# Kernel tuning notes

Hardware: AMD Instinct MI355X
Metric: run time of the kernel (lower is better)

## Reference

```python
import jax, jax.numpy as jnp
import numpy as np

B, S, D_IN, D_HID, D_OUT, PE_DIM = 8, 4096, 1024, 1024, 1024, 16


def sinusoidal_embeddings(batch_size, seq_len, dim):
    positions = jnp.arange(seq_len)[:, None].astype(jnp.float32)
    div_term = jnp.exp(jnp.arange(0, dim, 2).astype(jnp.float32) * (-jnp.log(10000.0) / dim))
    pe = jnp.zeros((seq_len, dim), dtype=jnp.float32)
    pe = pe.at[:, 0::2].set(jnp.sin(positions * div_term))
    pe = pe.at[:, 1::2].set(jnp.cos(positions * div_term))
    return jnp.broadcast_to(pe, (batch_size, seq_len, dim))


def setup_inputs() -> dict:
    key = jax.random.key(0)
    ks = jax.random.split(key, 8)
    d_cat = D_IN + PE_DIM
    # a_logit drawn so that sigmoid(a_logit) lands in the stable decay range [0.9, 0.999]
    u = jax.random.uniform(ks[1], (D_HID,), minval=0.9, maxval=0.999)
    a_logit = jnp.log(u) - jnp.log1p(-u)  # logit
    scale_in = 1.0 / np.sqrt(d_cat)
    scale_h = 1.0 / np.sqrt(D_HID)
    return {
        "x": jax.random.normal(ks[0], (B, S, D_IN), dtype=jnp.float32),
        "a_logit": a_logit.astype(jnp.float32),
        "W_dx": jax.random.normal(ks[2], (d_cat, D_OUT), dtype=jnp.float32) * scale_in,
        "b_dx": jnp.zeros((D_OUT,), dtype=jnp.float32),
        "W_in": jax.random.normal(ks[3], (d_cat, D_HID), dtype=jnp.float32) * scale_in,
        "b_in": jnp.zeros((D_HID,), dtype=jnp.float32),
        "W_out": jax.random.normal(ks[4], (D_HID, D_OUT), dtype=jnp.float32) * scale_h,
        "b_out": jnp.zeros((D_OUT,), dtype=jnp.float32),
    }


def reference(x, a_logit, W_dx, b_dx, W_in, b_in, W_out, b_out):
    batch, seq, _ = x.shape
    a = jax.nn.sigmoid(a_logit)  # (d_hidden,)
    # rnn_pos_embedding: concat 16-dim sinusoidal PE
    xc = jnp.concatenate([x, sinusoidal_embeddings(batch, seq, PE_DIM)], axis=-1)
    dx = xc @ W_dx + b_dx  # (B, S, d_out)
    u = xc @ W_in + b_in  # (B, S, d_hidden)
    # rnn_norm_input
    u = jnp.sqrt(1.0 - a ** 2) * u
    u = jnp.transpose(u, (1, 0, 2))  # (S, B, d_hidden)

    def step(h, xt):
        h = a * h + xt
        return h, h

    init = jnp.zeros((batch, a.shape[0]), dtype=x.dtype)
    _, h = jax.lax.scan(step, init, u)
    h = jnp.transpose(h, (1, 0, 2))  # (B, S, d_hidden)
    return (dx + h @ W_out + b_out) / 2
```

## Files before the change

kernel.cpp:

```cpp
#include <hip/hip_runtime.h>
#include <hip/hip_bf16.h>
#include <math.h>

#define B_DIM 8
#define S_DIM 4096
#define DIN   1024
#define DHID  1024
#define DOUT  1024
#define KCAT  1040
#define KC    1088
#define MTOT  (B_DIM*S_DIM)
#define NCHUNK 32
#define LCHUNK 128

typedef __attribute__((ext_vector_type(8))) short bf16x8;
typedef __attribute__((ext_vector_type(4))) float f32x4;
typedef __attribute__((ext_vector_type(4))) unsigned short u16x4;

__device__ __forceinline__ unsigned short f2bf(float f) {
  union { float f; unsigned u; } v; v.f = f;
  unsigned r = v.u + 0x7fffu + ((v.u >> 16) & 1u);
  return (unsigned short)(r >> 16);
}
__device__ __forceinline__ float bf2f(unsigned short h) {
  union { unsigned u; float f; } v; v.u = ((unsigned)h) << 16;
  return v.f;
}

#define GLOAD16(g, l)                                                         \
  __builtin_amdgcn_global_load_lds(                                           \
      (const __attribute__((address_space(1))) void*)(g),                     \
      (__attribute__((address_space(3))) void*)(l), 16, 0, 0)

#define BAR()   __builtin_amdgcn_s_barrier()
#define LGKM0() do { asm volatile("s_waitcnt lgkmcnt(0)" ::: "memory");       \
                     __builtin_amdgcn_sched_barrier(0); } while (0)


__global__ void prep_a_kernel(const float* __restrict__ logit,
                              float* __restrict__ avec, float* __restrict__ svec) {
  int d = blockIdx.x * 256 + threadIdx.x;
  if (d >= DHID) return;
  float a = 1.f / (1.f + expf(-logit[d]));
  avec[d] = a;
  svec[d] = sqrtf(fmaxf(0.f, 1.f - a * a));
}

__global__ __launch_bounds__(256) void transpose_cast_kernel(
    const float* __restrict__ W, unsigned short* __restrict__ Wt,
    int Ksrc, int KCdst) {
  __shared__ float tile[32][33];
  const int N = 1024;
  int kb = blockIdx.x * 32, nb = blockIdx.y * 32;
  int tx = threadIdx.x & 31, ty = threadIdx.x >> 5;
#pragma unroll
  for (int r = 0; r < 32; r += 8) {
    int k = kb + ty + r;
    tile[ty + r][tx] = (k < Ksrc) ? W[(size_t)k * N + nb + tx] : 0.f;
  }
  __syncthreads();
#pragma unroll
  for (int r = 0; r < 32; r += 8) {
    int n = nb + ty + r;
    Wt[(size_t)n * KCdst + kb + tx] = f2bf(tile[tx][ty + r]);
  }
}

__global__ __launch_bounds__(256) void build_xc_kernel(
    const float* __restrict__ x, unsigned short* __restrict__ xc) {
  int gid = blockIdx.x * 256 + threadIdx.x;
  if (gid >= MTOT * (KC / 4)) return;
  int row = gid / (KC / 4);
  int g = gid - row * (KC / 4);
  int col0 = g * 4;
  u16x4 val;
  if (col0 < DIN) {
    const float4 xv = *(const float4*)(x + (size_t)row * DIN + col0);
    val.x = f2bf(xv.x); val.y = f2bf(xv.y); val.z = f2bf(xv.z); val.w = f2bf(xv.w);
  } else {
    int t = row & (S_DIM - 1);
#pragma unroll
    for (int e = 0; e < 4; e++) {
      int col = col0 + e;
      float v = 0.f;
      if (col < KCAT) {
        int j = col - DIN;
        int i = j >> 1;
        float div = expf(-(float)i * 1.1512925465f);
        float arg = (float)t * div;
        v = (j & 1) ? cosf(arg) : sinf(arg);
      }
      val[e] = f2bf(v);
    }
  }
  *(u16x4*)(xc + (size_t)row * KC + col0) = val;
}


__device__ __forceinline__ bf16x8 frag(const unsigned short* hb, int row, int slot) {
  int ph = slot ^ (row & 7);
  return *(const bf16x8*)(hb + (size_t)row * 64 + ph * 8);
}

__device__ __forceinline__ void gemm_pipe2(
    const unsigned short* __restrict__ A,
    const unsigned short* __restrict__ Bt,
    int lda, int kt, int arow0, int brow0,
    unsigned short (*lA)[2][8192], unsigned short (*lB)[2][8192],
    f32x4 acc[8][4]) {
  const int tid = threadIdx.x;
  const int lane = tid & 63, w = tid >> 6;
  const int wrow = w >> 2, wcol = w & 3;
  const int rl = lane & 15, s = lane >> 4;

  const int c1 = tid, c2 = tid + 512;
  const int r1 = c1 >> 3, sl1 = (c1 & 7) ^ (r1 & 7);
  const int r2 = c2 >> 3, sl2 = (c2 & 7) ^ (r2 & 7);
  const unsigned short* pA1 = A + (size_t)(arow0 + r1) * lda + sl1 * 8;
  const unsigned short* pA2 = A + (size_t)(arow0 + r2) * lda + sl2 * 8;
  const unsigned short* pB1 = Bt + (size_t)(brow0 + r1) * lda + sl1 * 8;
  const unsigned short* pB2 = Bt + (size_t)(brow0 + r2) * lda + sl2 * 8;
  const size_t hstep = (size_t)128 * lda;

#define STG_A(t, h) do { size_t _o = (size_t)(t) * 64 + (size_t)(h) * hstep;  \
    int _b = (t) & 1;                                                         \
    GLOAD16(pA1 + _o, &lA[_b][h][(size_t)c1 * 8]);                            \
    GLOAD16(pA2 + _o, &lA[_b][h][(size_t)c2 * 8]); } while (0)
#define STG_B(t, h) do { size_t _o = (size_t)(t) * 64 + (size_t)(h) * hstep;  \
    int _b = (t) & 1;                                                         \
    GLOAD16(pB1 + _o, &lB[_b][h][(size_t)c1 * 8]);                            \
    GLOAD16(pB2 + _o, &lB[_b][h][(size_t)c2 * 8]); } while (0)

#define MFMA_Q(MH, NH, BB)                                                    \
  __builtin_amdgcn_s_setprio(1);                                              \
  _Pragma("unroll") for (int mq = 0; mq < 4; mq++)                            \
    _Pragma("unroll") for (int nq = 0; nq < 2; nq++)                          \
      _Pragma("unroll") for (int kk = 0; kk < 2; kk++)                        \
        acc[(MH)*4 + mq][(NH)*2 + nq] =                                       \
            __builtin_amdgcn_mfma_f32_16x16x32_bf16(                          \
                a[mq][kk], BB[nq][kk], acc[(MH)*4 + mq][(NH)*2 + nq], 0, 0, 0);\
  __builtin_amdgcn_s_setprio(0);

  STG_B(0, 0); STG_B(0, 1); STG_A(0, 0); STG_A(0, 1);
  STG_B(1, 0); STG_B(1, 1); STG_A(1, 0); STG_A(1, 1);
  asm volatile("s_waitcnt vmcnt(8)" ::: "memory");
  BAR();

  const int br = (wcol & 1) * 64;
  for (int t = 0; t < kt; ++t) {
    const bool st = (t + 2) < kt;
    const unsigned short* Ac = &lA[t & 1][wrow][0];
    const unsigned short* Bc = &lB[t & 1][wcol >> 1][0];
    bf16x8 a[4][2], b0[2][2], b1[2][2];

#pragma unroll
    for (int mq = 0; mq < 4; mq++)
#pragma unroll
      for (int kk = 0; kk < 2; kk++)
        a[mq][kk] = frag(Ac, mq * 16 + rl, kk * 4 + s);
#pragma unroll
    for (int nq = 0; nq < 2; nq++)
#pragma unroll
      for (int kk = 0; kk < 2; kk++)
        b0[nq][kk] = frag(Bc, br + nq * 16 + rl, kk * 4 + s);
    BAR(); LGKM0();
    MFMA_Q(0, 0, b0);
    BAR();

#pragma unroll
    for (int nq = 0; nq < 2; nq++)
#pragma unroll
      for (int kk = 0; kk < 2; kk++)
        b1[nq][kk] = frag(Bc, br + 32 + nq * 16 + rl, kk * 4 + s);
    BAR(); LGKM0();
    MFMA_Q(0, 1, b1);
    BAR();

#pragma unroll
    for (int mq = 0; mq < 4; mq++)
#pragma unroll
      for (int kk = 0; kk < 2; kk++)
        a[mq][kk] = frag(Ac, 64 + mq * 16 + rl, kk * 4 + s);
    if (st) { STG_B(t + 2, 0); STG_B(t + 2, 1); }
    BAR(); LGKM0();
    MFMA_Q(1, 1, b1);
    BAR();

    if (st) { STG_A(t + 2, 0); STG_A(t + 2, 1); }
    BAR();
    MFMA_Q(1, 0, b0);
    if (st) { asm volatile("s_waitcnt vmcnt(8)" ::: "memory"); }
    else    { asm volatile("s_waitcnt vmcnt(0)" ::: "memory"); }
    BAR();
  }
#undef STG_A
#undef STG_B
#undef MFMA_Q
}

__global__ __launch_bounds__(512, 2) void gemm_u_kernel(
    const unsigned short* __restrict__ xc, const unsigned short* __restrict__ Wtin,
    const float* __restrict__ b_in, const float* __restrict__ svec,
    unsigned short* __restrict__ u) {
  __shared__ __align__(16) unsigned short lA[2][2][8192];
  __shared__ __align__(16) unsigned short lB[2][2][8192];
  f32x4 acc[8][4];
  const f32x4 z = {0.f, 0.f, 0.f, 0.f};
#pragma unroll
  for (int i = 0; i < 8; i++)
#pragma unroll
    for (int n = 0; n < 4; n++) acc[i][n] = z;

  int bid = blockIdx.x;
  int swz = (bid & 7) * 64 + (bid >> 3);
  int bcol = swz >> 7, brow = swz & 127;

  gemm_pipe2(xc, Wtin, KC, KC / 64, brow * 256, bcol * 256, lA, lB, acc);

  const int lane = threadIdx.x & 63, w = threadIdx.x >> 6;
  const int wrow = w >> 2, wcol = w & 3;
  const int rl = lane & 15, s = lane >> 4;
  const int colb = bcol * 256 + wcol * 64 + rl;
  const int rowb = brow * 256 + wrow * 128 + s * 4;
#pragma unroll
  for (int n = 0; n < 4; n++) {
    int col = colb + n * 16;
    float bi = b_in[col], sv = svec[col];
#pragma unroll
    for (int i = 0; i < 8; i++) {
#pragma unroll
      for (int r = 0; r < 4; r++) {
        int row = rowb + i * 16 + r;
        u[(size_t)row * DHID + col] = f2bf((acc[i][n][r] + bi) * sv);
      }
    }
  }
}

__global__ __launch_bounds__(512, 2) void gemm_out_kernel(
    const unsigned short* __restrict__ xc, const unsigned short* __restrict__ Wtdx,
    const unsigned short* __restrict__ h, const unsigned short* __restrict__ Wtout,
    const float* __restrict__ b_dx, const float* __restrict__ b_out,
    float* __restrict__ out) {
  __shared__ __align__(16) unsigned short lA[2][2][8192];
  __shared__ __align__(16) unsigned short lB[2][2][8192];
  f32x4 acc[8][4];
  const f32x4 z = {0.f, 0.f, 0.f, 0.f};
#pragma unroll
  for (int i = 0; i < 8; i++)
#pragma unroll
    for (int n = 0; n < 4; n++) acc[i][n] = z;

  int bid = blockIdx.x;
  int swz = (bid & 7) * 64 + (bid >> 3);
  int bcol = swz >> 7, brow = swz & 127;

  gemm_pipe2(xc, Wtdx, KC, KC / 64, brow * 256, bcol * 256, lA, lB, acc);
  gemm_pipe2(h, Wtout, DHID, DHID / 64, brow * 256, bcol * 256, lA, lB, acc);

  const int lane = threadIdx.x & 63, w = threadIdx.x >> 6;
  const int wrow = w >> 2, wcol = w & 3;
  const int rl = lane & 15, s = lane >> 4;
  const int colb = bcol * 256 + wcol * 64 + rl;
  const int rowb = brow * 256 + wrow * 128 + s * 4;
#pragma unroll
  for (int n = 0; n < 4; n++) {
    int col = colb + n * 16;
    float bb = b_dx[col] + b_out[col];
#pragma unroll
    for (int i = 0; i < 8; i++) {
#pragma unroll
      for (int r = 0; r < 4; r++) {
        int row = rowb + i * 16 + r;
        out[(size_t)row * DOUT + col] = 0.5f * (acc[i][n][r] + bb);
      }
    }
  }
}


__global__ __launch_bounds__(256) void scan1_kernel(
    const float* __restrict__ avec, unsigned short* __restrict__ uh,
    float* __restrict__ carry) {
  int b = blockIdx.x >> 5, c = blockIdx.x & 31;
  int d0 = threadIdx.x * 4;
  float4 a4 = *(const float4*)(avec + d0);
  unsigned short* p = uh + ((size_t)(b * S_DIM + c * LCHUNK)) * DHID + d0;
  float h0 = 0.f, h1 = 0.f, h2 = 0.f, h3 = 0.f;
#pragma unroll 4
  for (int t = 0; t < LCHUNK; t++) {
    u16x4 v = *(u16x4*)(p + (size_t)t * DHID);
    h0 = fmaf(a4.x, h0, bf2f(v.x));
    h1 = fmaf(a4.y, h1, bf2f(v.y));
    h2 = fmaf(a4.z, h2, bf2f(v.z));
    h3 = fmaf(a4.w, h3, bf2f(v.w));
    v.x = f2bf(h0); v.y = f2bf(h1); v.z = f2bf(h2); v.w = f2bf(h3);
    *(u16x4*)(p + (size_t)t * DHID) = v;
  }
  float4 cv = {h0, h1, h2, h3};
  *(float4*)(carry + ((size_t)b * NCHUNK + c) * DHID + d0) = cv;
}

__global__ __launch_bounds__(256) void scan2_kernel(
    const float* __restrict__ avec, const float* __restrict__ carry,
    float* __restrict__ Hprev) {
  int gid = blockIdx.x * 256 + threadIdx.x;
  int b = gid >> 10, d = gid & 1023;
  float a = avec[d];
  float aL = a;
#pragma unroll
  for (int i = 0; i < 7; i++) aL *= aL;
  float H = 0.f;
#pragma unroll
  for (int c = 0; c < NCHUNK; c++) {
    size_t idx = ((size_t)b * NCHUNK + c) * DHID + d;
    Hprev[idx] = H;
    H = aL * H + carry[idx];
  }
}

__global__ __launch_bounds__(256) void scan3_kernel(
    const float* __restrict__ avec, unsigned short* __restrict__ uh,
    const float* __restrict__ Hprev) {
  int b = blockIdx.x >> 5, c = blockIdx.x & 31;
  int d0 = threadIdx.x * 4;
  float4 Hp = *(const float4*)(Hprev + ((size_t)b * NCHUNK + c) * DHID + d0);
  if (Hp.x == 0.f && Hp.y == 0.f && Hp.z == 0.f && Hp.w == 0.f) return;
  float4 a4 = *(const float4*)(avec + d0);
  float p0 = a4.x * Hp.x, p1 = a4.y * Hp.y, p2 = a4.z * Hp.z, p3 = a4.w * Hp.w;
  unsigned short* p = uh + ((size_t)(b * S_DIM + c * LCHUNK)) * DHID + d0;
#pragma unroll 4
  for (int t = 0; t < LCHUNK; t++) {
    u16x4 v = *(u16x4*)(p + (size_t)t * DHID);
    v.x = f2bf(bf2f(v.x) + p0);
    v.y = f2bf(bf2f(v.y) + p1);
    v.z = f2bf(bf2f(v.z) + p2);
    v.w = f2bf(bf2f(v.w) + p3);
    *(u16x4*)(p + (size_t)t * DHID) = v;
    p0 *= a4.x; p1 *= a4.y; p2 *= a4.z; p3 *= a4.w;
  }
}


extern "C" void kernel_launch(void* const* d_in, const int* in_sizes, int n_in,
                              void* d_out, int out_size, void* d_ws, size_t ws_size,
                              hipStream_t stream) {
  const float* x       = (const float*)d_in[0];
  const float* a_logit = (const float*)d_in[1];
  const float* W_dx    = (const float*)d_in[2];
  const float* b_dx    = (const float*)d_in[3];
  const float* W_in    = (const float*)d_in[4];
  const float* b_in    = (const float*)d_in[5];
  const float* W_out   = (const float*)d_in[6];
  const float* b_out   = (const float*)d_in[7];
  float* out = (float*)d_out;

  char* ws = (char*)d_ws;
  size_t off = 0;
  auto alloc = [&](size_t bytes) {
    void* p = ws + off;
    off += (bytes + 255) & ~(size_t)255;
    return p;
  };
  unsigned short* xc    = (unsigned short*)alloc((size_t)MTOT * KC * 2);
  unsigned short* Wtdx  = (unsigned short*)alloc((size_t)DOUT * KC * 2);
  unsigned short* Wtin  = (unsigned short*)alloc((size_t)DHID * KC * 2);
  unsigned short* Wtout = (unsigned short*)alloc((size_t)DOUT * DHID * 2);
  unsigned short* uh    = (unsigned short*)alloc((size_t)MTOT * DHID * 2);
  float* carry = (float*)alloc((size_t)B_DIM * NCHUNK * DHID * 4);
  float* Hprev = (float*)alloc((size_t)B_DIM * NCHUNK * DHID * 4);
  float* avec  = (float*)alloc(DHID * 4);
  float* svec  = (float*)alloc(DHID * 4);
  (void)ws_size; (void)in_sizes; (void)n_in; (void)out_size;

  prep_a_kernel<<<4, 256, 0, stream>>>(a_logit, avec, svec);
  transpose_cast_kernel<<<dim3(KC / 32, 32), 256, 0, stream>>>(W_dx, Wtdx, KCAT, KC);
  transpose_cast_kernel<<<dim3(KC / 32, 32), 256, 0, stream>>>(W_in, Wtin, KCAT, KC);
  transpose_cast_kernel<<<dim3(32, 32), 256, 0, stream>>>(W_out, Wtout, DHID, DHID);
  build_xc_kernel<<<(MTOT * (KC / 4) + 255) / 256, 256, 0, stream>>>(x, xc);

  gemm_u_kernel<<<512, 512, 0, stream>>>(xc, Wtin, b_in, svec, uh);

  scan1_kernel<<<B_DIM * NCHUNK, 256, 0, stream>>>(avec, uh, carry);
  scan2_kernel<<<32, 256, 0, stream>>>(avec, carry, Hprev);
  scan3_kernel<<<B_DIM * NCHUNK, 256, 0, stream>>>(avec, uh, Hprev);

  gemm_out_kernel<<<512, 512, 0, stream>>>(xc, Wtdx, uh, Wtout, b_dx, b_out, out);
}
```

Before: 339.6 us.

## Restructure GEMM main loop with register prefetch and fused dual-GEMM pipeline

Result: slower. 356.1 us (+4.8%).

```diff
diff --git a/kernel.cpp b/kernel.cpp
--- a/kernel.cpp
+++ b/kernel.cpp
@@ -31,10 +31,6 @@
   __builtin_amdgcn_global_load_lds(                                           \
       (const __attribute__((address_space(1))) void*)(g),                     \
       (__attribute__((address_space(3))) void*)(l), 16, 0, 0)
-
-#define BAR()   __builtin_amdgcn_s_barrier()
-#define LGKM0() do { asm volatile("s_waitcnt lgkmcnt(0)" ::: "memory");       \
-                     __builtin_amdgcn_sched_barrier(0); } while (0)
 
 
 __global__ void prep_a_kernel(const float* __restrict__ logit,
@@ -102,100 +98,114 @@
   return *(const bf16x8*)(hb + (size_t)row * 64 + ph * 8);
 }
 
-__device__ __forceinline__ void gemm_pipe2(
-    const unsigned short* __restrict__ A,
-    const unsigned short* __restrict__ Bt,
-    int lda, int kt, int arow0, int brow0,
+#define READ_A(dst, base, roff)                                               \
+  _Pragma("unroll") for (int mq = 0; mq < 4; mq++)                            \
+    _Pragma("unroll") for (int kk = 0; kk < 2; kk++)                          \
+      dst[mq][kk] = frag(base, (roff) + mq * 16 + rl, kk * 4 + s);
+
+#define READ_B(dst, base, roff)                                               \
+  _Pragma("unroll") for (int nq = 0; nq < 2; nq++)                            \
+    _Pragma("unroll") for (int kk = 0; kk < 2; kk++)                          \
+      dst[nq][kk] = frag(base, (roff) + nq * 16 + rl, kk * 4 + s);
+
+#define MFMA_Q(MH, NH, AA, BB)                                                \
+  __builtin_amdgcn_s_setprio(1);                                              \
+  _Pragma("unroll") for (int mq = 0; mq < 4; mq++)                            \
+    _Pragma("unroll") for (int nq = 0; nq < 2; nq++)                          \
+      _Pragma("unroll") for (int kk = 0; kk < 2; kk++)                        \
+        acc[(MH)*4 + mq][(NH)*2 + nq] =                                       \
+            __builtin_amdgcn_mfma_f32_16x16x32_bf16(                          \
+                AA[mq][kk], BB[nq][kk], acc[(MH)*4 + mq][(NH)*2 + nq], 0,0,0);\
+  __builtin_amdgcn_s_setprio(0);
+
+__device__ __forceinline__ void gemm_pipe3(
+    const unsigned short* __restrict__ A0p, const unsigned short* __restrict__ B0p,
+    int lda0, int kt0,
+    const unsigned short* __restrict__ A1p, const unsigned short* __restrict__ B1p,
+    int lda1, int kt1,
+    int arow0, int brow0,
     unsigned short (*lA)[2][8192], unsigned short (*lB)[2][8192],
     f32x4 acc[8][4]) {
   const int tid = threadIdx.x;
   const int lane = tid & 63, w = tid >> 6;
   const int wrow = w >> 2, wcol = w & 3;
   const int rl = lane & 15, s = lane >> 4;
+  const int br = (wcol & 1) * 64;
+  const int kt = kt0 + kt1;
 
   const int c1 = tid, c2 = tid + 512;
   const int r1 = c1 >> 3, sl1 = (c1 & 7) ^ (r1 & 7);
   const int r2 = c2 >> 3, sl2 = (c2 & 7) ^ (r2 & 7);
-  const unsigned short* pA1 = A + (size_t)(arow0 + r1) * lda + sl1 * 8;
-  const unsigned short* pA2 = A + (size_t)(arow0 + r2) * lda + sl2 * 8;
-  const unsigned short* pB1 = Bt + (size_t)(brow0 + r1) * lda + sl1 * 8;
-  const unsigned short* pB2 = Bt + (size_t)(brow0 + r2) * lda + sl2 * 8;
-  const size_t hstep = (size_t)128 * lda;
-
-#define STG_A(t, h) do { size_t _o = (size_t)(t) * 64 + (size_t)(h) * hstep;  \
-    int _b = (t) & 1;                                                         \
-    GLOAD16(pA1 + _o, &lA[_b][h][(size_t)c1 * 8]);                            \
-    GLOAD16(pA2 + _o, &lA[_b][h][(size_t)c2 * 8]); } while (0)
-#define STG_B(t, h) do { size_t _o = (size_t)(t) * 64 + (size_t)(h) * hstep;  \
-    int _b = (t) & 1;                                                         \
-    GLOAD16(pB1 + _o, &lB[_b][h][(size_t)c1 * 8]);                            \
-    GLOAD16(pB2 + _o, &lB[_b][h][(size_t)c2 * 8]); } while (0)
-
-#define MFMA_Q(MH, NH, BB)                                                    \
-  __builtin_amdgcn_s_setprio(1);                                              \
-  _Pragma("unroll") for (int mq = 0; mq < 4; mq++)                            \
-    _Pragma("unroll") for (int nq = 0; nq < 2; nq++)                          \
-      _Pragma("unroll") for (int kk = 0; kk < 2; kk++)                        \
-        acc[(MH)*4 + mq][(NH)*2 + nq] =                                       \
-            __builtin_amdgcn_mfma_f32_16x16x32_bf16(                          \
-                a[mq][kk], BB[nq][kk], acc[(MH)*4 + mq][(NH)*2 + nq], 0, 0, 0);\
-  __builtin_amdgcn_s_setprio(0);
-
-  STG_B(0, 0); STG_B(0, 1); STG_A(0, 0); STG_A(0, 1);
-  STG_B(1, 0); STG_B(1, 1); STG_A(1, 0); STG_A(1, 1);
+  const unsigned short* gA00 = A0p + (size_t)(arow0 + r1) * lda0 + sl1 * 8;
+  const unsigned short* gA01 = A0p + (size_t)(arow0 + r2) * lda0 + sl2 * 8;
+  const unsigned short* gB00 = B0p + (size_t)(brow0 + r1) * lda0 + sl1 * 8;
+  const unsigned short* gB01 = B0p + (size_t)(brow0 + r2) * lda0 + sl2 * 8;
+  const unsigned short* gA10 = A1p + (size_t)(arow0 + r1) * lda1 + sl1 * 8;
+  const unsigned short* gA11 = A1p + (size_t)(arow0 + r2) * lda1 + sl2 * 8;
+  const unsigned short* gB10 = B1p + (size_t)(brow0 + r1) * lda1 + sl1 * 8;
+  const unsigned short* gB11 = B1p + (size_t)(brow0 + r2) * lda1 + sl2 * 8;
+  const size_t hstep0 = (size_t)128 * lda0, hstep1 = (size_t)128 * lda1;
+
+#define STAGE(tt) do {                                                        \
+    int _sg = (tt) >= kt0;                                                    \
+    size_t _ko = (size_t)((tt) - (_sg ? kt0 : 0)) * 64;                       \
+    const unsigned short* _a0 = (_sg ? gA10 : gA00) + _ko;                    \
+    const unsigned short* _a1 = (_sg ? gA11 : gA01) + _ko;                    \
+    const unsigned short* _b0 = (_sg ? gB10 : gB00) + _ko;                    \
+    const unsigned short* _b1 = (_sg ? gB11 : gB01) + _ko;                    \
+    size_t _hs = _sg ? hstep1 : hstep0;                                       \
+    int _bb = (tt) & 1;                                                       \
+    GLOAD16(_a0,       &lA[_bb][0][(size_t)c1 * 8]);                          \
+    GLOAD16(_a1,       &lA[_bb][0][(size_t)c2 * 8]);                          \
+    GLOAD16(_a0 + _hs, &lA[_bb][1][(size_t)c1 * 8]);                          \
+    GLOAD16(_a1 + _hs, &lA[_bb][1][(size_t)c2 * 8]);                          \
+    GLOAD16(_b0,       &lB[_bb][0][(size_t)c1 * 8]);                          \
+    GLOAD16(_b1,       &lB[_bb][0][(size_t)c2 * 8]);                          \
+    GLOAD16(_b0 + _hs, &lB[_bb][1][(size_t)c1 * 8]);                          \
+    GLOAD16(_b1 + _hs, &lB[_bb][1][(size_t)c2 * 8]);                          \
+  } while (0)
+
+  STAGE(0); STAGE(1);
   asm volatile("s_waitcnt vmcnt(8)" ::: "memory");
-  BAR();
-
-  const int br = (wcol & 1) * 64;
+  __builtin_amdgcn_s_barrier();
+  __builtin_amdgcn_sched_barrier(0);
+
+  bf16x8 a0[4][2], a1[4][2], b0[2][2], b1[2][2];
+  {
+    const unsigned short* Ac = &lA[0][wrow][0];
+    const unsigned short* Bc = &lB[0][wcol >> 1][0];
+    READ_A(a0, Ac, 0);
+    READ_B(b0, Bc, br);
+  }
+
   for (int t = 0; t < kt; ++t) {
     const bool st = (t + 2) < kt;
     const unsigned short* Ac = &lA[t & 1][wrow][0];
     const unsigned short* Bc = &lB[t & 1][wcol >> 1][0];
-    bf16x8 a[4][2], b0[2][2], b1[2][2];
-
-#pragma unroll
-    for (int mq = 0; mq < 4; mq++)
-#pragma unroll
-      for (int kk = 0; kk < 2; kk++)
-        a[mq][kk] = frag(Ac, mq * 16 + rl, kk * 4 + s);
-#pragma unroll
-    for (int nq = 0; nq < 2; nq++)
-#pragma unroll
-      for (int kk = 0; kk < 2; kk++)
-        b0[nq][kk] = frag(Bc, br + nq * 16 + rl, kk * 4 + s);
-    BAR(); LGKM0();
-    MFMA_Q(0, 0, b0);
-    BAR();
-
-#pragma unroll
-    for (int nq = 0; nq < 2; nq++)
-#pragma unroll
-      for (int kk = 0; kk < 2; kk++)
-        b1[nq][kk] = frag(Bc, br + 32 + nq * 16 + rl, kk * 4 + s);
-    BAR(); LGKM0();
-    MFMA_Q(0, 1, b1);
-    BAR();
-
-#pragma unroll
-    for (int mq = 0; mq < 4; mq++)
-#pragma unroll
-      for (int kk = 0; kk < 2; kk++)
-        a[mq][kk] = frag(Ac, 64 + mq * 16 + rl, kk * 4 + s);
-    if (st) { STG_B(t + 2, 0); STG_B(t + 2, 1); }
-    BAR(); LGKM0();
-    MFMA_Q(1, 1, b1);
-    BAR();
-
-    if (st) { STG_A(t + 2, 0); STG_A(t + 2, 1); }
-    BAR();
-    MFMA_Q(1, 0, b0);
-    if (st) { asm volatile("s_waitcnt vmcnt(8)" ::: "memory"); }
-    else    { asm volatile("s_waitcnt vmcnt(0)" ::: "memory"); }
-    BAR();
-  }
-#undef STG_A
-#undef STG_B
-#undef MFMA_Q
+    READ_A(a1, Ac, 64);
+    READ_B(b1, Bc, br + 32);
+    MFMA_Q(0, 0, a0, b0);
+    MFMA_Q(1, 1, a1, b1);
+    __builtin_amdgcn_s_barrier();
+    MFMA_Q(0, 1, a0, b1);
+    __builtin_amdgcn_sched_barrier(0);
+    if (st) {
+      STAGE(t + 2);
+      asm volatile("s_waitcnt vmcnt(8)" ::: "memory");
+    } else {
+      asm volatile("s_waitcnt vmcnt(0)" ::: "memory");
+    }
+    __builtin_amdgcn_s_barrier();
+    __builtin_amdgcn_sched_barrier(0);
+    MFMA_Q(1, 0, a1, b0);
+    if (t + 1 < kt) {
+      const unsigned short* An = &lA[(t + 1) & 1][wrow][0];
+      const unsigned short* Bn = &lB[(t + 1) & 1][wcol >> 1][0];
+      READ_A(a0, An, 0);
+      READ_B(b0, Bn, br);
+    }
+  }
+#undef STAGE
 }
 
 __global__ __launch_bounds__(512, 2) void gemm_u_kernel(
@@ -215,7 +225,8 @@
   int swz = (bid & 7) * 64 + (bid >> 3);
   int bcol = swz >> 7, brow = swz & 127;
 
-  gemm_pipe2(xc, Wtin, KC, KC / 64, brow * 256, bcol * 256, lA, lB, acc);
+  gemm_pipe3(xc, Wtin, KC, KC / 64, xc, Wtin, KC, 0,
+             brow * 256, bcol * 256, lA, lB, acc);
 
   const int lane = threadIdx.x & 63, w = threadIdx.x >> 6;
   const int wrow = w >> 2, wcol = w & 3;
@@ -255,8 +266,8 @@
   int swz = (bid & 7) * 64 + (bid >> 3);
   int bcol = swz >> 7, brow = swz & 127;
 
-  gemm_pipe2(xc, Wtdx, KC, KC / 64, brow * 256, bcol * 256, lA, lB, acc);
-  gemm_pipe2(h, Wtout, DHID, DHID / 64, brow * 256, bcol * 256, lA, lB, acc);
+  gemm_pipe3(xc, Wtdx, KC, KC / 64, h, Wtout, DHID, DHID / 64,
+             brow * 256, bcol * 256, lA, lB, acc);
 
   const int lane = threadIdx.x & 63, w = threadIdx.x >> 6;
   const int wrow = w >> 2, wcol = w & 3;
```

## Load B fragments directly from global and triple-buffer A tiles in LDS

Applied to the files above, without the earlier changes.

Result: slower. 453.3 us (+33.5%).

```diff
diff --git a/kernel.cpp b/kernel.cpp
--- a/kernel.cpp
+++ b/kernel.cpp
@@ -31,10 +31,6 @@
   __builtin_amdgcn_global_load_lds(                                           \
       (const __attribute__((address_space(1))) void*)(g),                     \
       (__attribute__((address_space(3))) void*)(l), 16, 0, 0)
-
-#define BAR()   __builtin_amdgcn_s_barrier()
-#define LGKM0() do { asm volatile("s_waitcnt lgkmcnt(0)" ::: "memory");       \
-                     __builtin_amdgcn_sched_barrier(0); } while (0)
 
 
 __global__ void prep_a_kernel(const float* __restrict__ logit,
@@ -102,108 +98,97 @@
   return *(const bf16x8*)(hb + (size_t)row * 64 + ph * 8);
 }
 
-__device__ __forceinline__ void gemm_pipe2(
-    const unsigned short* __restrict__ A,
-    const unsigned short* __restrict__ Bt,
-    int lda, int kt, int arow0, int brow0,
-    unsigned short (*lA)[2][8192], unsigned short (*lB)[2][8192],
-    f32x4 acc[8][4]) {
+template <int NSEG>
+__device__ __forceinline__ void gemm_pipe(
+    const unsigned short* __restrict__ A0p, const unsigned short* __restrict__ B0p,
+    int lda0, int kt0,
+    const unsigned short* __restrict__ A1p, const unsigned short* __restrict__ B1p,
+    int lda1, int kt1,
+    int arow0, int bcol0,
+    unsigned short* lA, f32x4 acc[8][4]) {
   const int tid = threadIdx.x;
   const int lane = tid & 63, w = tid >> 6;
   const int wrow = w >> 2, wcol = w & 3;
   const int rl = lane & 15, s = lane >> 4;
-
-  const int c1 = tid, c2 = tid + 512;
-  const int r1 = c1 >> 3, sl1 = (c1 & 7) ^ (r1 & 7);
-  const int r2 = c2 >> 3, sl2 = (c2 & 7) ^ (r2 & 7);
-  const unsigned short* pA1 = A + (size_t)(arow0 + r1) * lda + sl1 * 8;
-  const unsigned short* pA2 = A + (size_t)(arow0 + r2) * lda + sl2 * 8;
-  const unsigned short* pB1 = Bt + (size_t)(brow0 + r1) * lda + sl1 * 8;
-  const unsigned short* pB2 = Bt + (size_t)(brow0 + r2) * lda + sl2 * 8;
-  const size_t hstep = (size_t)128 * lda;
-
-#define STG_A(t, h) do { size_t _o = (size_t)(t) * 64 + (size_t)(h) * hstep;  \
-    int _b = (t) & 1;                                                         \
-    GLOAD16(pA1 + _o, &lA[_b][h][(size_t)c1 * 8]);                            \
-    GLOAD16(pA2 + _o, &lA[_b][h][(size_t)c2 * 8]); } while (0)
-#define STG_B(t, h) do { size_t _o = (size_t)(t) * 64 + (size_t)(h) * hstep;  \
-    int _b = (t) & 1;                                                         \
-    GLOAD16(pB1 + _o, &lB[_b][h][(size_t)c1 * 8]);                            \
-    GLOAD16(pB2 + _o, &lB[_b][h][(size_t)c2 * 8]); } while (0)
-
-#define MFMA_Q(MH, NH, BB)                                                    \
-  __builtin_amdgcn_s_setprio(1);                                              \
-  _Pragma("unroll") for (int mq = 0; mq < 4; mq++)                            \
-    _Pragma("unroll") for (int nq = 0; nq < 2; nq++)                          \
-      _Pragma("unroll") for (int kk = 0; kk < 2; kk++)                        \
-        acc[(MH)*4 + mq][(NH)*2 + nq] =                                       \
-            __builtin_amdgcn_mfma_f32_16x16x32_bf16(                          \
-                a[mq][kk], BB[nq][kk], acc[(MH)*4 + mq][(NH)*2 + nq], 0, 0, 0);\
-  __builtin_amdgcn_s_setprio(0);
-
-  STG_B(0, 0); STG_B(0, 1); STG_A(0, 0); STG_A(0, 1);
-  STG_B(1, 0); STG_B(1, 1); STG_A(1, 0); STG_A(1, 1);
-  asm volatile("s_waitcnt vmcnt(8)" ::: "memory");
-  BAR();
-
-  const int br = (wcol & 1) * 64;
+  const int kt = (NSEG == 2) ? (kt0 + kt1) : kt0;
+
+  const int r1 = tid >> 3;
+  const int sl1 = (tid & 7) ^ (r1 & 7);
+  const unsigned short* pA0 = A0p + (size_t)(arow0 + r1) * lda0 + sl1 * 8;
+  const unsigned short* pA1 = (NSEG == 2)
+      ? (A1p + (size_t)(arow0 + r1) * lda1 + sl1 * 8) : pA0;
+  const size_t q0 = (size_t)64 * lda0, q1 = (size_t)64 * lda1;
+
+  const unsigned short* gB0 = B0p + (size_t)(bcol0 + wcol * 64 + rl) * lda0 + s * 8;
+  const unsigned short* gB1 = (NSEG == 2)
+      ? (B1p + (size_t)(bcol0 + wcol * 64 + rl) * lda1 + s * 8) : gB0;
+
+  auto stage = [&](int tt) {
+    const unsigned short* pa = pA0;
+    size_t qq = q0;
+    int rel = tt;
+    if (NSEG == 2 && tt >= kt0) { pa = pA1; qq = q1; rel = tt - kt0; }
+    const unsigned short* src = pa + (size_t)rel * 64;
+    unsigned short* dst = lA + (tt % 3) * 16384 + (size_t)tid * 8;
+#pragma unroll
+    for (int jj = 0; jj < 4; jj++)
+      GLOAD16(src + (size_t)jj * qq, dst + (size_t)jj * 4096);
+  };
+
+  stage(0); stage(1);
+  asm volatile("s_waitcnt vmcnt(4)" ::: "memory");
+  __builtin_amdgcn_s_barrier();
+  __builtin_amdgcn_sched_barrier(0);
+
   for (int t = 0; t < kt; ++t) {
-    const bool st = (t + 2) < kt;
-    const unsigned short* Ac = &lA[t & 1][wrow][0];
-    const unsigned short* Bc = &lB[t & 1][wcol >> 1][0];
-    bf16x8 a[4][2], b0[2][2], b1[2][2];
-
-#pragma unroll
-    for (int mq = 0; mq < 4; mq++)
+    const bool st2 = (t + 2) < kt;
+    const unsigned short* gBt;
+    size_t nstr;
+    if (NSEG == 2 && t >= kt0) { gBt = gB1 + (size_t)(t - kt0) * 64; nstr = (size_t)16 * lda1; }
+    else                       { gBt = gB0 + (size_t)t * 64;         nstr = (size_t)16 * lda0; }
+    bf16x8 bf[4][2];
+#pragma unroll
+    for (int n = 0; n < 4; n++)
 #pragma unroll
       for (int kk = 0; kk < 2; kk++)
-        a[mq][kk] = frag(Ac, mq * 16 + rl, kk * 4 + s);
-#pragma unroll
-    for (int nq = 0; nq < 2; nq++)
-#pragma unroll
-      for (int kk = 0; kk < 2; kk++)
-        b0[nq][kk] = frag(Bc, br + nq * 16 + rl, kk * 4 + s);
-    BAR(); LGKM0();
-    MFMA_Q(0, 0, b0);
-    BAR();
-
-#pragma unroll
-    for (int nq = 0; nq < 2; nq++)
-#pragma unroll
-      for (int kk = 0; kk < 2; kk++)
-        b1[nq][kk] = frag(Bc, br + 32 + nq * 16 + rl, kk * 4 + s);
-    BAR(); LGKM0();
-    MFMA_Q(0, 1, b1);
-    BAR();
-
-#pragma unroll
-    for (int mq = 0; mq < 4; mq++)
-#pragma unroll
-      for (int kk = 0; kk < 2; kk++)
-        a[mq][kk] = frag(Ac, 64 + mq * 16 + rl, kk * 4 + s);
-    if (st) { STG_B(t + 2, 0); STG_B(t + 2, 1); }
-    BAR(); LGKM0();
-    MFMA_Q(1, 1, b1);
-    BAR();
-
-    if (st) { STG_A(t + 2, 0); STG_A(t + 2, 1); }
-    BAR();
-    MFMA_Q(1, 0, b0);
-    if (st) { asm volatile("s_waitcnt vmcnt(8)" ::: "memory"); }
-    else    { asm volatile("s_waitcnt vmcnt(0)" ::: "memory"); }
-    BAR();
-  }
-#undef STG_A
-#undef STG_B
-#undef MFMA_Q
+        bf[n][kk] = *(const bf16x8*)(gBt + (size_t)n * nstr + kk * 32);
+    __builtin_amdgcn_sched_barrier(0);
+    if (st2) stage(t + 2);
+    __builtin_amdgcn_sched_barrier(0);
+
+    const unsigned short* Ac = lA + (t % 3) * 16384;
+    bf16x8 af[8];
+#pragma unroll
+    for (int m = 0; m < 8; m++) af[m] = frag(Ac, wrow * 128 + m * 16 + rl, s);
+    __builtin_amdgcn_s_setprio(1);
+#pragma unroll
+    for (int m = 0; m < 8; m++)
+#pragma unroll
+      for (int n = 0; n < 4; n++)
+        acc[m][n] = __builtin_amdgcn_mfma_f32_16x16x32_bf16(af[m], bf[n][0], acc[m][n], 0, 0, 0);
+    __builtin_amdgcn_s_setprio(0);
+#pragma unroll
+    for (int m = 0; m < 8; m++) af[m] = frag(Ac, wrow * 128 + m * 16 + rl, 4 + s);
+    __builtin_amdgcn_s_setprio(1);
+#pragma unroll
+    for (int m = 0; m < 8; m++)
+#pragma unroll
+      for (int n = 0; n < 4; n++)
+        acc[m][n] = __builtin_amdgcn_mfma_f32_16x16x32_bf16(af[m], bf[n][1], acc[m][n], 0, 0, 0);
+    __builtin_amdgcn_s_setprio(0);
+
+    if (st2) asm volatile("s_waitcnt vmcnt(4)" ::: "memory");
+    else     asm volatile("s_waitcnt vmcnt(0)" ::: "memory");
+    __builtin_amdgcn_s_barrier();
+    __builtin_amdgcn_sched_barrier(0);
+  }
 }
 
 __global__ __launch_bounds__(512, 2) void gemm_u_kernel(
     const unsigned short* __restrict__ xc, const unsigned short* __restrict__ Wtin,
     const float* __restrict__ b_in, const float* __restrict__ svec,
     unsigned short* __restrict__ u) {
-  __shared__ __align__(16) unsigned short lA[2][2][8192];
-  __shared__ __align__(16) unsigned short lB[2][2][8192];
+  __shared__ __align__(16) unsigned short lA[3 * 16384];
   f32x4 acc[8][4];
   const f32x4 z = {0.f, 0.f, 0.f, 0.f};
 #pragma unroll
@@ -215,7 +200,8 @@
   int swz = (bid & 7) * 64 + (bid >> 3);
   int bcol = swz >> 7, brow = swz & 127;
 
-  gemm_pipe2(xc, Wtin, KC, KC / 64, brow * 256, bcol * 256, lA, lB, acc);
+  gemm_pipe<1>(xc, Wtin, KC, KC / 64, xc, Wtin, KC, 0,
+               brow * 256, bcol * 256, lA, acc);
 
   const int lane = threadIdx.x & 63, w = threadIdx.x >> 6;
   const int wrow = w >> 2, wcol = w & 3;
@@ -242,8 +228,7 @@
     const unsigned short* __restrict__ h, const unsigned short* __restrict__ Wtout,
     const float* __restrict__ b_dx, const float* __restrict__ b_out,
     float* __restrict__ out) {
-  __shared__ __align__(16) unsigned short lA[2][2][8192];
-  __shared__ __align__(16) unsigned short lB[2][2][8192];
+  __shared__ __align__(16) unsigned short lA[3 * 16384];
   f32x4 acc[8][4];
   const f32x4 z = {0.f, 0.f, 0.f, 0.f};
 #pragma unroll
@@ -255,8 +240,8 @@
   int swz = (bid & 7) * 64 + (bid >> 3);
   int bcol = swz >> 7, brow = swz & 127;
 
-  gemm_pipe2(xc, Wtdx, KC, KC / 64, brow * 256, bcol * 256, lA, lB, acc);
-  gemm_pipe2(h, Wtout, DHID, DHID / 64, brow * 256, bcol * 256, lA, lB, acc);
+  gemm_pipe<2>(xc, Wtdx, KC, KC / 64, h, Wtout, DHID, DHID / 64,
+               brow * 256, bcol * 256, lA, acc);
 
   const int lane = threadIdx.x & 63, w = threadIdx.x >> 6;
   const int wrow = w >> 2, wcol = w & 3;
```

## Fold positional-embedding projection into GEMM epilogues and restage pipeline loads

Applied to the files above, without the earlier changes.

Result: slower. 412.8 us (+21.6%).

```diff
diff --git a/kernel.cpp b/kernel.cpp
--- a/kernel.cpp
+++ b/kernel.cpp
@@ -7,8 +7,7 @@
 #define DIN   1024
 #define DHID  1024
 #define DOUT  1024
-#define KCAT  1040
-#define KC    1088
+#define LDA   1024
 #define MTOT  (B_DIM*S_DIM)
 #define NCHUNK 32
 #define LCHUNK 128
@@ -16,6 +15,7 @@
 typedef __attribute__((ext_vector_type(8))) short bf16x8;
 typedef __attribute__((ext_vector_type(4))) float f32x4;
 typedef __attribute__((ext_vector_type(4))) unsigned short u16x4;
+typedef __attribute__((ext_vector_type(8))) unsigned short u16x8;
 
 __device__ __forceinline__ unsigned short f2bf(float f) {
   union { float f; unsigned u; } v; v.f = f;
@@ -47,53 +47,53 @@
 }
 
 __global__ __launch_bounds__(256) void transpose_cast_kernel(
-    const float* __restrict__ W, unsigned short* __restrict__ Wt,
-    int Ksrc, int KCdst) {
+    const float* __restrict__ W, unsigned short* __restrict__ Wt) {
   __shared__ float tile[32][33];
   const int N = 1024;
   int kb = blockIdx.x * 32, nb = blockIdx.y * 32;
   int tx = threadIdx.x & 31, ty = threadIdx.x >> 5;
 #pragma unroll
-  for (int r = 0; r < 32; r += 8) {
-    int k = kb + ty + r;
-    tile[ty + r][tx] = (k < Ksrc) ? W[(size_t)k * N + nb + tx] : 0.f;
-  }
+  for (int r = 0; r < 32; r += 8)
+    tile[ty + r][tx] = W[(size_t)(kb + ty + r) * N + nb + tx];
   __syncthreads();
 #pragma unroll
-  for (int r = 0; r < 32; r += 8) {
-    int n = nb + ty + r;
-    Wt[(size_t)n * KCdst + kb + tx] = f2bf(tile[tx][ty + r]);
-  }
-}
-
-__global__ __launch_bounds__(256) void build_xc_kernel(
-    const float* __restrict__ x, unsigned short* __restrict__ xc) {
-  int gid = blockIdx.x * 256 + threadIdx.x;
-  if (gid >= MTOT * (KC / 4)) return;
-  int row = gid / (KC / 4);
-  int g = gid - row * (KC / 4);
-  int col0 = g * 4;
-  u16x4 val;
-  if (col0 < DIN) {
-    const float4 xv = *(const float4*)(x + (size_t)row * DIN + col0);
-    val.x = f2bf(xv.x); val.y = f2bf(xv.y); val.z = f2bf(xv.z); val.w = f2bf(xv.w);
-  } else {
-    int t = row & (S_DIM - 1);
-#pragma unroll
-    for (int e = 0; e < 4; e++) {
-      int col = col0 + e;
-      float v = 0.f;
-      if (col < KCAT) {
-        int j = col - DIN;
-        int i = j >> 1;
-        float div = expf(-(float)i * 1.1512925465f);
-        float arg = (float)t * div;
-        v = (j & 1) ? cosf(arg) : sinf(arg);
-      }
-      val[e] = f2bf(v);
-    }
-  }
-  *(u16x4*)(xc + (size_t)row * KC + col0) = val;
+  for (int r = 0; r < 32; r += 8)
+    Wt[(size_t)(nb + ty + r) * N + kb + tx] = f2bf(tile[tx][ty + r]);
+}
+
+__global__ __launch_bounds__(256) void pew_kernel(const float* __restrict__ W,
+                                                  float* __restrict__ PEW) {
+  __shared__ float pe[16];
+  int t = blockIdx.x;
+  if (threadIdx.x < 16) {
+    int j = threadIdx.x, i = j >> 1;
+    float div = expf(-(float)i * 1.1512925465f);
+    float arg = (float)t * div;
+    pe[j] = (j & 1) ? cosf(arg) : sinf(arg);
+  }
+  __syncthreads();
+  int col0 = threadIdx.x * 4;
+  float a0 = 0.f, a1 = 0.f, a2 = 0.f, a3 = 0.f;
+#pragma unroll
+  for (int j = 0; j < 16; j++) {
+    const float4 wv = *(const float4*)(W + (size_t)(1024 + j) * 1024 + col0);
+    float p = pe[j];
+    a0 = fmaf(p, wv.x, a0); a1 = fmaf(p, wv.y, a1);
+    a2 = fmaf(p, wv.z, a2); a3 = fmaf(p, wv.w, a3);
+  }
+  float4 o = {a0, a1, a2, a3};
+  *(float4*)(PEW + (size_t)t * 1024 + col0) = o;
+}
+
+__global__ __launch_bounds__(256) void cast_kernel(const float* __restrict__ x,
+                                                   unsigned short* __restrict__ xb) {
+  size_t i = ((size_t)blockIdx.x * 256 + threadIdx.x) * 8;
+  float4 v0 = *(const float4*)(x + i);
+  float4 v1 = *(const float4*)(x + i + 4);
+  u16x8 o;
+  o[0] = f2bf(v0.x); o[1] = f2bf(v0.y); o[2] = f2bf(v0.z); o[3] = f2bf(v0.w);
+  o[4] = f2bf(v1.x); o[5] = f2bf(v1.y); o[6] = f2bf(v1.z); o[7] = f2bf(v1.w);
+  *(u16x8*)(xb + i) = o;
 }
 
 
@@ -102,106 +102,120 @@
   return *(const bf16x8*)(hb + (size_t)row * 64 + ph * 8);
 }
 
-__device__ __forceinline__ void gemm_pipe2(
-    const unsigned short* __restrict__ A,
-    const unsigned short* __restrict__ Bt,
-    int lda, int kt, int arow0, int brow0,
+#define READ_A4(dst, base, roff)                                              \
+  _Pragma("unroll") for (int mq = 0; mq < 4; mq++)                            \
+    _Pragma("unroll") for (int kk = 0; kk < 2; kk++)                          \
+      dst[mq][kk] = frag(base, (roff) + mq * 16 + rl, kk * 4 + s);
+
+#define READ_B2(dst, base, roff)                                              \
+  _Pragma("unroll") for (int nq = 0; nq < 2; nq++)                            \
+    _Pragma("unroll") for (int kk = 0; kk < 2; kk++)                          \
+      dst[nq][kk] = frag(base, (roff) + nq * 16 + rl, kk * 4 + s);
+
+#define MFMA_Q(MH, NH, AA, BB)                                                \
+  __builtin_amdgcn_s_setprio(1);                                              \
+  _Pragma("unroll") for (int mq = 0; mq < 4; mq++)                            \
+    _Pragma("unroll") for (int nq = 0; nq < 2; nq++)                          \
+      _Pragma("unroll") for (int kk = 0; kk < 2; kk++)                        \
+        acc[(MH)*4 + mq][(NH)*2 + nq] =                                       \
+            __builtin_amdgcn_mfma_f32_16x16x32_bf16(                          \
+                AA[mq][kk], BB[nq][kk], acc[(MH)*4 + mq][(NH)*2 + nq], 0,0,0);\
+  __builtin_amdgcn_s_setprio(0);
+
+template <int NSEG>
+__device__ __forceinline__ void gemm_pipe4(
+    const unsigned short* __restrict__ A0p, const unsigned short* __restrict__ B0p,
+    int kt0,
+    const unsigned short* __restrict__ A1p, const unsigned short* __restrict__ B1p,
+    int kt1,
+    int arow0, int bcol0,
     unsigned short (*lA)[2][8192], unsigned short (*lB)[2][8192],
     f32x4 acc[8][4]) {
   const int tid = threadIdx.x;
   const int lane = tid & 63, w = tid >> 6;
   const int wrow = w >> 2, wcol = w & 3;
   const int rl = lane & 15, s = lane >> 4;
+  const int br = (wcol & 1) * 64;
+  const int kt = (NSEG == 2) ? (kt0 + kt1) : kt0;
 
   const int c1 = tid, c2 = tid + 512;
   const int r1 = c1 >> 3, sl1 = (c1 & 7) ^ (r1 & 7);
   const int r2 = c2 >> 3, sl2 = (c2 & 7) ^ (r2 & 7);
-  const unsigned short* pA1 = A + (size_t)(arow0 + r1) * lda + sl1 * 8;
-  const unsigned short* pA2 = A + (size_t)(arow0 + r2) * lda + sl2 * 8;
-  const unsigned short* pB1 = Bt + (size_t)(brow0 + r1) * lda + sl1 * 8;
-  const unsigned short* pB2 = Bt + (size_t)(brow0 + r2) * lda + sl2 * 8;
-  const size_t hstep = (size_t)128 * lda;
-
-#define STG_A(t, h) do { size_t _o = (size_t)(t) * 64 + (size_t)(h) * hstep;  \
-    int _b = (t) & 1;                                                         \
-    GLOAD16(pA1 + _o, &lA[_b][h][(size_t)c1 * 8]);                            \
-    GLOAD16(pA2 + _o, &lA[_b][h][(size_t)c2 * 8]); } while (0)
-#define STG_B(t, h) do { size_t _o = (size_t)(t) * 64 + (size_t)(h) * hstep;  \
-    int _b = (t) & 1;                                                         \
-    GLOAD16(pB1 + _o, &lB[_b][h][(size_t)c1 * 8]);                            \
-    GLOAD16(pB2 + _o, &lB[_b][h][(size_t)c2 * 8]); } while (0)
-
-#define MFMA_Q(MH, NH, BB)                                                    \
-  __builtin_amdgcn_s_setprio(1);                                              \
-  _Pragma("unroll") for (int mq = 0; mq < 4; mq++)                            \
-    _Pragma("unroll") for (int nq = 0; nq < 2; nq++)                          \
-      _Pragma("unroll") for (int kk = 0; kk < 2; kk++)                        \
-        acc[(MH)*4 + mq][(NH)*2 + nq] =                                       \
-            __builtin_amdgcn_mfma_f32_16x16x32_bf16(                          \
-                a[mq][kk], BB[nq][kk], acc[(MH)*4 + mq][(NH)*2 + nq], 0, 0, 0);\
-  __builtin_amdgcn_s_setprio(0);
-
-  STG_B(0, 0); STG_B(0, 1); STG_A(0, 0); STG_A(0, 1);
-  STG_B(1, 0); STG_B(1, 1); STG_A(1, 0); STG_A(1, 1);
-  asm volatile("s_waitcnt vmcnt(8)" ::: "memory");
+  const unsigned short* gAa0 = A0p + (size_t)(arow0 + r1) * LDA + sl1 * 8;
+  const unsigned short* gAb0 = A0p + (size_t)(arow0 + r2) * LDA + sl2 * 8;
+  const unsigned short* gBa0 = B0p + (size_t)(bcol0 + r1) * LDA + sl1 * 8;
+  const unsigned short* gBb0 = B0p + (size_t)(bcol0 + r2) * LDA + sl2 * 8;
+  const unsigned short* gAa1 = gAa0; const unsigned short* gAb1 = gAb0;
+  const unsigned short* gBa1 = gBa0; const unsigned short* gBb1 = gBb0;
+  if (NSEG == 2) {
+    gAa1 = A1p + (size_t)(arow0 + r1) * LDA + sl1 * 8;
+    gAb1 = A1p + (size_t)(arow0 + r2) * LDA + sl2 * 8;
+    gBa1 = B1p + (size_t)(bcol0 + r1) * LDA + sl1 * 8;
+    gBb1 = B1p + (size_t)(bcol0 + r2) * LDA + sl2 * 8;
+  }
+  const size_t hstep = (size_t)128 * LDA;
+
+  auto stg_a = [&](int tt, int h) {
+    const unsigned short* pa = gAa0; const unsigned short* pb = gAb0; int rel = tt;
+    if (NSEG == 2 && tt >= kt0) { pa = gAa1; pb = gAb1; rel = tt - kt0; }
+    size_t o = (size_t)rel * 64 + (size_t)h * hstep;
+    GLOAD16(pa + o, &lA[tt & 1][h][(size_t)c1 * 8]);
+    GLOAD16(pb + o, &lA[tt & 1][h][(size_t)c2 * 8]);
+  };
+  auto stg_b = [&](int tt, int h) {
+    const unsigned short* pa = gBa0; const unsigned short* pb = gBb0; int rel = tt;
+    if (NSEG == 2 && tt >= kt0) { pa = gBa1; pb = gBb1; rel = tt - kt0; }
+    size_t o = (size_t)rel * 64 + (size_t)h * hstep;
+    GLOAD16(pa + o, &lB[tt & 1][h][(size_t)c1 * 8]);
+    GLOAD16(pb + o, &lB[tt & 1][h][(size_t)c2 * 8]);
+  };
+
+  stg_a(0, 0); stg_a(0, 1); stg_b(0, 0); stg_b(0, 1);
+  stg_b(1, 0); stg_b(1, 1);
+  asm volatile("s_waitcnt vmcnt(4)" ::: "memory");
   BAR();
-
-  const int br = (wcol & 1) * 64;
+  __builtin_amdgcn_sched_barrier(0);
+
   for (int t = 0; t < kt; ++t) {
-    const bool st = (t + 2) < kt;
     const unsigned short* Ac = &lA[t & 1][wrow][0];
     const unsigned short* Bc = &lB[t & 1][wcol >> 1][0];
-    bf16x8 a[4][2], b0[2][2], b1[2][2];
-
-#pragma unroll
-    for (int mq = 0; mq < 4; mq++)
-#pragma unroll
-      for (int kk = 0; kk < 2; kk++)
-        a[mq][kk] = frag(Ac, mq * 16 + rl, kk * 4 + s);
-#pragma unroll
-    for (int nq = 0; nq < 2; nq++)
-#pragma unroll
-      for (int kk = 0; kk < 2; kk++)
-        b0[nq][kk] = frag(Bc, br + nq * 16 + rl, kk * 4 + s);
+    bf16x8 alo[4][2], ahi[4][2], blo[2][2], bhi[2][2];
+
+    READ_A4(alo, Ac, 0);
+    READ_B2(blo, Bc, br);
+    if (t + 1 < kt) stg_a(t + 1, 0);
     BAR(); LGKM0();
-    MFMA_Q(0, 0, b0);
+    MFMA_Q(0, 0, alo, blo);
     BAR();
 
-#pragma unroll
-    for (int nq = 0; nq < 2; nq++)
-#pragma unroll
-      for (int kk = 0; kk < 2; kk++)
-        b1[nq][kk] = frag(Bc, br + 32 + nq * 16 + rl, kk * 4 + s);
+    READ_B2(bhi, Bc, br + 32);
+    if (t + 1 < kt) stg_a(t + 1, 1);
     BAR(); LGKM0();
-    MFMA_Q(0, 1, b1);
+    MFMA_Q(0, 1, alo, bhi);
     BAR();
 
-#pragma unroll
-    for (int mq = 0; mq < 4; mq++)
-#pragma unroll
-      for (int kk = 0; kk < 2; kk++)
-        a[mq][kk] = frag(Ac, 64 + mq * 16 + rl, kk * 4 + s);
-    if (st) { STG_B(t + 2, 0); STG_B(t + 2, 1); }
+    READ_A4(ahi, Ac, 64);
+    if (t + 2 < kt) stg_b(t + 2, 0);
     BAR(); LGKM0();
-    MFMA_Q(1, 1, b1);
+    MFMA_Q(1, 1, ahi, bhi);
     BAR();
 
-    if (st) { STG_A(t + 2, 0); STG_A(t + 2, 1); }
+    if (t + 2 < kt) {
+      stg_b(t + 2, 1);
+      asm volatile("s_waitcnt vmcnt(4)" ::: "memory");
+    } else {
+      asm volatile("s_waitcnt vmcnt(0)" ::: "memory");
+    }
     BAR();
-    MFMA_Q(1, 0, b0);
-    if (st) { asm volatile("s_waitcnt vmcnt(8)" ::: "memory"); }
-    else    { asm volatile("s_waitcnt vmcnt(0)" ::: "memory"); }
-    BAR();
-  }
-#undef STG_A
-#undef STG_B
-#undef MFMA_Q
+    __builtin_amdgcn_sched_barrier(0);
+    MFMA_Q(1, 0, ahi, blo);
+  }
 }
 
 __global__ __launch_bounds__(512, 2) void gemm_u_kernel(
-    const unsigned short* __restrict__ xc, const unsigned short* __restrict__ Wtin,
+    const unsigned short* __restrict__ xb, const unsigned short* __restrict__ Wtin,
     const float* __restrict__ b_in, const float* __restrict__ svec,
-    unsigned short* __restrict__ u) {
+    const float* __restrict__ PEWin, unsigned short* __restrict__ u) {
   __shared__ __align__(16) unsigned short lA[2][2][8192];
   __shared__ __align__(16) unsigned short lB[2][2][8192];
   f32x4 acc[8][4];
@@ -215,7 +229,7 @@
   int swz = (bid & 7) * 64 + (bid >> 3);
   int bcol = swz >> 7, brow = swz & 127;
 
-  gemm_pipe2(xc, Wtin, KC, KC / 64, brow * 256, bcol * 256, lA, lB, acc);
+  gemm_pipe4<1>(xb, Wtin, LDA / 64, xb, Wtin, 0, brow * 256, bcol * 256, lA, lB, acc);
 
   const int lane = threadIdx.x & 63, w = threadIdx.x >> 6;
   const int wrow = w >> 2, wcol = w & 3;
@@ -231,17 +245,18 @@
 #pragma unroll
       for (int r = 0; r < 4; r++) {
         int row = rowb + i * 16 + r;
-        u[(size_t)row * DHID + col] = f2bf((acc[i][n][r] + bi) * sv);
+        float peb = PEWin[(size_t)((row & (S_DIM - 1)) << 10) + col];
+        u[(size_t)row * DHID + col] = f2bf((acc[i][n][r] + bi + peb) * sv);
       }
     }
   }
 }
 
 __global__ __launch_bounds__(512, 2) void gemm_out_kernel(
-    const unsigned short* __restrict__ xc, const unsigned short* __restrict__ Wtdx,
+    const unsigned short* __restrict__ xb, const unsigned short* __restrict__ Wtdx,
     const unsigned short* __restrict__ h, const unsigned short* __restrict__ Wtout,
     const float* __restrict__ b_dx, const float* __restrict__ b_out,
-    float* __restrict__ out) {
+    const float* __restrict__ PEWdx, float* __restrict__ out) {
   __shared__ __align__(16) unsigned short lA[2][2][8192];
   __shared__ __align__(16) unsigned short lB[2][2][8192];
   f32x4 acc[8][4];
@@ -255,8 +270,8 @@
   int swz = (bid & 7) * 64 + (bid >> 3);
   int bcol = swz >> 7, brow = swz & 127;
 
-  gemm_pipe2(xc, Wtdx, KC, KC / 64, brow * 256, bcol * 256, lA, lB, acc);
-  gemm_pipe2(h, Wtout, DHID, DHID / 64, brow * 256, bcol * 256, lA, lB, acc);
+  gemm_pipe4<2>(xb, Wtdx, LDA / 64, h, Wtout, LDA / 64, brow * 256, bcol * 256,
+                lA, lB, acc);
 
   const int lane = threadIdx.x & 63, w = threadIdx.x >> 6;
   const int wrow = w >> 2, wcol = w & 3;
@@ -272,7 +287,8 @@
 #pragma unroll
       for (int r = 0; r < 4; r++) {
         int row = rowb + i * 16 + r;
-        out[(size_t)row * DOUT + col] = 0.5f * (acc[i][n][r] + bb);
+        float peb = PEWdx[(size_t)((row & (S_DIM - 1)) << 10) + col];
+        out[(size_t)row * DOUT + col] = 0.5f * (acc[i][n][r] + bb + peb);
       }
     }
   }
@@ -362,11 +378,13 @@
     off += (bytes + 255) & ~(size_t)255;
     return p;
   };
-  unsigned short* xc    = (unsigned short*)alloc((size_t)MTOT * KC * 2);
-  unsigned short* Wtdx  = (unsigned short*)alloc((size_t)DOUT * KC * 2);
-  unsigned short* Wtin  = (unsigned short*)alloc((size_t)DHID * KC * 2);
-  unsigned short* Wtout = (unsigned short*)alloc((size_t)DOUT * DHID * 2);
-  unsigned short* uh    = (unsigned short*)alloc((size_t)MTOT * DHID * 2);
+  unsigned short* xb    = (unsigned short*)alloc((size_t)MTOT * 1024 * 2);
+  unsigned short* Wtdx  = (unsigned short*)alloc((size_t)1024 * 1024 * 2);
+  unsigned short* Wtin  = (unsigned short*)alloc((size_t)1024 * 1024 * 2);
+  unsigned short* Wtout = (unsigned short*)alloc((size_t)1024 * 1024 * 2);
+  unsigned short* uh    = (unsigned short*)alloc((size_t)MTOT * 1024 * 2);
+  float* PEWdx = (float*)alloc((size_t)S_DIM * 1024 * 4);
+  float* PEWin = (float*)alloc((size_t)S_DIM * 1024 * 4);
   float* carry = (float*)alloc((size_t)B_DIM * NCHUNK * DHID * 4);
   float* Hprev = (float*)alloc((size_t)B_DIM * NCHUNK * DHID * 4);
   float* avec  = (float*)alloc(DHID * 4);
@@ -374,16 +392,19 @@
   (void)ws_size; (void)in_sizes; (void)n_in; (void)out_size;
 
   prep_a_kernel<<<4, 256, 0, stream>>>(a_logit, avec, svec);
-  transpose_cast_kernel<<<dim3(KC / 32, 32), 256, 0, stream>>>(W_dx, Wtdx, KCAT, KC);
-  transpose_cast_kernel<<<dim3(KC / 32, 32), 256, 0, stream>>>(W_in, Wtin, KCAT, KC);
-  transpose_cast_kernel<<<dim3(32, 32), 256, 0, stream>>>(W_out, Wtout, DHID, DHID);
-  build_xc_kernel<<<(MTOT * (KC / 4) + 255) / 256, 256, 0, stream>>>(x, xc);
-
-  gemm_u_kernel<<<512, 512, 0, stream>>>(xc, Wtin, b_in, svec, uh);
+  transpose_cast_kernel<<<dim3(32, 32), 256, 0, stream>>>(W_dx, Wtdx);
+  transpose_cast_kernel<<<dim3(32, 32), 256, 0, stream>>>(W_in, Wtin);
+  transpose_cast_kernel<<<dim3(32, 32), 256, 0, stream>>>(W_out, Wtout);
+  pew_kernel<<<S_DIM, 256, 0, stream>>>(W_dx, PEWdx);
+  pew_kernel<<<S_DIM, 256, 0, stream>>>(W_in, PEWin);
+  cast_kernel<<<MTOT * 1024 / 8 / 256, 256, 0, stream>>>(x, xb);
+
+  gemm_u_kernel<<<512, 512, 0, stream>>>(xb, Wtin, b_in, svec, PEWin, uh);
 
   scan1_kernel<<<B_DIM * NCHUNK, 256, 0, stream>>>(avec, uh, carry);
   scan2_kernel<<<32, 256, 0, stream>>>(avec, carry, Hprev);
   scan3_kernel<<<B_DIM * NCHUNK, 256, 0, stream>>>(avec, uh, Hprev);
 
-  gemm_out_kernel<<<512, 512, 0, stream>>>(xc, Wtdx, uh, Wtout, b_dx, b_out, out);
-}
+  gemm_out_kernel<<<512, 512, 0, stream>>>(xb, Wtdx, uh, Wtout, b_dx, b_out,
+                                           PEWdx, out);
+}
```
